# Kernel optimization log

Hardware: AMD Instinct MI355X
Metric: run time of the kernel (lower is better)

The kernel has to match this reference:

```python
import jax, jax.numpy as jnp
import numpy as np

D_MODEL = 1024
NUM_HEADS = 16
HEAD_DIM = D_MODEL // NUM_HEADS


def setup_inputs() -> dict:
    key = jax.random.key(0)
    ks = jax.random.split(key, 11)
    B, S = 2, 2048
    s = 1.0 / np.sqrt(D_MODEL)
    inp = {
        "query": jax.random.normal(ks[0], (B, S, D_MODEL), jnp.float32),
        "key": jax.random.normal(ks[1], (B, S, D_MODEL), jnp.float32),
        "value": jax.random.normal(ks[2], (B, S, D_MODEL), jnp.float32),
        "Wq": jax.random.normal(ks[3], (D_MODEL, D_MODEL), jnp.float32) * s,
        "bq": jnp.zeros((D_MODEL,), jnp.float32),
        "Wk": jax.random.normal(ks[4], (D_MODEL, D_MODEL), jnp.float32) * s,
        "bk": jnp.zeros((D_MODEL,), jnp.float32),
        "Wv": jax.random.normal(ks[5], (D_MODEL, D_MODEL), jnp.float32) * s,
        "bv": jnp.zeros((D_MODEL,), jnp.float32),
        "Wo": jax.random.normal(ks[6], (D_MODEL, D_MODEL), jnp.float32) * s,
        "bo": jnp.zeros((D_MODEL,), jnp.float32),
    }
    return inp


def _split_heads(x):
    B, S, _ = x.shape
    return x.reshape(B, S, NUM_HEADS, HEAD_DIM).transpose(0, 2, 1, 3)  # [B,H,S,d]


def reference(query, key, value, Wq, bq, Wk, bk, Wv, bv, Wo, bo):
    Q = _split_heads(query @ Wq.T + bq)
    K = _split_heads(key @ Wk.T + bk)
    V = _split_heads(value @ Wv.T + bv)
    scale = 1.0 / jnp.sqrt(jnp.asarray(HEAD_DIM, jnp.float32))
    scores = jnp.einsum("bhqd,bhkd->bhqk", Q, K) * scale  # [B,H,S,S]
    weights = jax.nn.softmax(scores, axis=-1)
    attn = jnp.einsum("bhqk,bhkd->bhqd", weights, V)
    B, H, S, d = attn.shape
    attn = attn.transpose(0, 2, 1, 3).reshape(B, S, H * d)
    return attn @ Wo.T + bo
```

## Files before the change

kernel.cpp:

```cpp
#include <hip/hip_runtime.h>
#include <hip/hip_bf16.h>


typedef unsigned short u16;
typedef __attribute__((ext_vector_type(8))) short short8;
typedef __attribute__((ext_vector_type(4))) float floatx4;

__device__ __forceinline__ float bf2f(u16 x) {
  return __uint_as_float(((unsigned)x) << 16);
}
__device__ __forceinline__ u16 f2bf(float f) {
  unsigned x = __float_as_uint(f);
  return (u16)((x + 0x7fffu + ((x >> 16) & 1u)) >> 16);
}
__device__ __forceinline__ ushort2 pk_bf16(float a, float b) {
  __hip_bfloat162 h2 = __float22bfloat162_rn(make_float2(a, b));
  ushort2 u;
  __builtin_memcpy(&u, &h2, 4);
  return u;
}
#if __has_builtin(__builtin_amdgcn_exp2f)
#define EXP2(x) __builtin_amdgcn_exp2f(x)
#else
#define EXP2(x) exp2f(x)
#endif
__device__ __forceinline__ void gll16(const u16* g, u16* lds) {
  __builtin_amdgcn_global_load_lds((const __attribute__((address_space(1))) void*)g,
                                   (__attribute__((address_space(3))) void*)lds,
                                   16, 0, 0);
}

__global__ __launch_bounds__(256) void cvt_kernel(
    const float* __restrict__ q, const float* __restrict__ k, const float* __restrict__ v,
    const float* __restrict__ wq, const float* __restrict__ wk,
    const float* __restrict__ wv, const float* __restrict__ wo,
    const float* __restrict__ bq, const float* __restrict__ bk,
    const float* __restrict__ bv, const float* __restrict__ bo,
    u16* __restrict__ ws) {
  const int i4 = (blockIdx.x * 256 + threadIdx.x) * 4;
  const float* src;
  u16* dst;
  int local;
  if (i4 < 4194304)        { src = q;  dst = ws;            local = i4; }
  else if (i4 < 8388608)   { src = k;  dst = ws + 4194304;  local = i4 - 4194304; }
  else if (i4 < 12582912)  { src = v;  dst = ws + 8388608;  local = i4 - 8388608; }
  else if (i4 < 13631488)  { src = wq; dst = ws + 12582912; local = i4 - 12582912; }
  else if (i4 < 14680064)  { src = wk; dst = ws + 13631488; local = i4 - 13631488; }
  else if (i4 < 15728640)  { src = wv; dst = ws + 14680064; local = i4 - 14680064; }
  else if (i4 < 16777216)  { src = wo; dst = ws + 15728640; local = i4 - 15728640; }
  else if (i4 < 16778240)  { src = bq; dst = ws + 16777216; local = i4 - 16777216; }
  else if (i4 < 16779264)  { src = bk; dst = ws + 16779264; local = i4 - 16778240; }
  else if (i4 < 16780288)  { src = bv; dst = ws + 16781312; local = i4 - 16779264; }
  else                     { src = bo; dst = ws + 16783360; local = i4 - 16780288; }
  const float4 f = *(const float4*)(src + local);
  ushort4 o;
  o.x = f2bf(f.x); o.y = f2bf(f.y); o.z = f2bf(f.z); o.w = f2bf(f.w);
  *(ushort4*)(dst + local) = o;
}

template <int MTILE>
__device__ __forceinline__ void gemm_tile(
    const u16* __restrict__ X, const u16* __restrict__ W,
    const u16* __restrict__ bias, u16* __restrict__ out16, float* __restrict__ out32,
    int row0, int col0, int mode, float oscale, u16* As, u16* Bs) {
  constexpr int NI = MTILE / 32;
  constexpr int ABUF = MTILE * 32;
  const int tid = threadIdx.x;
  const int w = tid >> 6, l = tid & 63;
  const int lan = l & 15, quad = l >> 4;
  const int wm = w & 1, wn = w >> 1;

  floatx4 acc[NI][4];
#pragma unroll
  for (int i = 0; i < NI; ++i)
#pragma unroll
    for (int j = 0; j < 4; ++j) acc[i][j] = (floatx4)0.0f;

  const int r0 = tid >> 2, kq0 = tid & 3;
  const int r1 = (tid + 256) >> 2;
  const int woff = w * 512;
  const u16* Xa0 = X + (size_t)(row0 + r0) * 1024 + kq0 * 8;
  const u16* Xa1 = X + (size_t)(row0 + (MTILE == 128 ? r1 : r0)) * 1024 + kq0 * 8;
  const u16* Wb0 = W + (size_t)(col0 + r0) * 1024 + kq0 * 8;
  const u16* Wb1 = W + (size_t)(col0 + r1) * 1024 + kq0 * 8;

#define STAGE(buf, kt)                                           \
  do {                                                           \
    gll16(Xa0 + (kt) * 32, As + (buf) * ABUF + woff);            \
    if (MTILE == 128)                                            \
      gll16(Xa1 + (kt) * 32, As + (buf) * ABUF + 2048 + woff);   \
    gll16(Wb0 + (kt) * 32, Bs + (buf) * 4096 + woff);            \
    gll16(Wb1 + (kt) * 32, Bs + (buf) * 4096 + 2048 + woff);     \
  } while (0)

  STAGE(0, 0);
  int cur = 0;
  for (int kt = 0; kt < 32; ++kt) {
    if (kt < 31) {
      const int nb = cur == 2 ? 0 : cur + 1;
      STAGE(nb, kt + 1);
      if (MTILE == 128)
        __asm__ volatile("s_waitcnt vmcnt(4)" ::: "memory");
      else
        __asm__ volatile("s_waitcnt vmcnt(3)" ::: "memory");
    } else {
      __asm__ volatile("s_waitcnt vmcnt(0)" ::: "memory");
    }
    __builtin_amdgcn_s_barrier();

    const u16* Ab = As + cur * ABUF;
    const u16* Bb = Bs + cur * 4096;
    short8 af[NI], bfr[4];
#pragma unroll
    for (int i = 0; i < NI; ++i)
      af[i] = *(const short8*)(Ab + (wm * (MTILE / 2) + i * 16 + lan) * 32 + quad * 8);
#pragma unroll
    for (int j = 0; j < 4; ++j)
      bfr[j] = *(const short8*)(Bb + (wn * 64 + j * 16 + lan) * 32 + quad * 8);
#pragma unroll
    for (int i = 0; i < NI; ++i)
#pragma unroll
      for (int j = 0; j < 4; ++j)
        acc[i][j] = __builtin_amdgcn_mfma_f32_16x16x32_bf16(af[i], bfr[j], acc[i][j], 0, 0, 0);
    cur = cur == 2 ? 0 : cur + 1;
  }
#undef STAGE

#pragma unroll
  for (int i = 0; i < NI; ++i) {
    const int mb = row0 + wm * (MTILE / 2) + i * 16 + quad * 4;
#pragma unroll
    for (int j = 0; j < 4; ++j) {
      const int n = col0 + wn * 64 + j * 16 + lan;
      const float bv = bf2f(bias[n]);
      if (mode == 0) {
#pragma unroll
        for (int r = 0; r < 4; ++r)
          out16[(size_t)(mb + r) * 1024 + n] = f2bf((acc[i][j][r] + bv) * oscale);
      } else if (mode == 1) {
        const int b = mb >> 11;
        const int h = n >> 6, dd = n & 63;
        u16* base = out16 + (size_t)((b * 16 + h) * 64 + dd) * 2048;
        const int s0 = mb & 2047;
        const int k0 = s0 & 63;
        const int sp0 = (s0 & ~63) | (((k0 >> 4) & 1) << 5) | (((k0 >> 2) & 3) << 3) |
                        (((k0 >> 5) & 1) << 2);
        ushort4 ov;
        ov.x = f2bf(acc[i][j][0] + bv);
        ov.y = f2bf(acc[i][j][1] + bv);
        ov.z = f2bf(acc[i][j][2] + bv);
        ov.w = f2bf(acc[i][j][3] + bv);
        *(ushort4*)(base + sp0) = ov;
      } else {
#pragma unroll
        for (int r = 0; r < 4; ++r)
          out32[(size_t)(mb + r) * 1024 + n] = acc[i][j][r] + bv;
      }
    }
  }
}

__global__ __launch_bounds__(256) void qkv_kernel(
    const u16* __restrict__ xq, const u16* __restrict__ xk, const u16* __restrict__ xv,
    const u16* __restrict__ Wq, const u16* __restrict__ Wk, const u16* __restrict__ Wv,
    const u16* __restrict__ bq, const u16* __restrict__ bk, const u16* __restrict__ bv,
    u16* __restrict__ Qo, u16* __restrict__ Ko, u16* __restrict__ Vto) {
  __shared__ __align__(16) u16 As[3 * 4096];
  __shared__ __align__(16) u16 Bs[3 * 4096];
  const int bx = blockIdx.x;
  const int xcd = bx & 7;
  const int j = bx >> 3;
  const int c = j & 7;
  const int gidx = j >> 3;
  const int g = gidx * 8 + xcd;
  const int which = g >> 5;
  const int tile_m = g & 31;
  const int col0 = c * 128;
  const u16* X = which == 0 ? xq : (which == 1 ? xk : xv);
  const u16* W = which == 0 ? Wq : (which == 1 ? Wk : Wv);
  const u16* bias = which == 0 ? bq : (which == 1 ? bk : bv);
  u16* out = which == 0 ? Qo : (which == 1 ? Ko : Vto);
  const float C = 0.125f * 1.4426950408889634f;
  gemm_tile<128>(X, W, bias, out, nullptr, tile_m * 128, col0, which == 2 ? 1 : 0,
                 which == 0 ? C : 1.0f, As, Bs);
}

__global__ __launch_bounds__(256) void proj_kernel(
    const u16* __restrict__ X, const u16* __restrict__ W,
    const u16* __restrict__ bias, float* __restrict__ out) {
  __shared__ __align__(16) u16 As[3 * 2048];
  __shared__ __align__(16) u16 Bs[3 * 4096];
  const int bx = blockIdx.x;
  const int xcd = bx & 7;
  const int j = bx >> 3;
  const int c = j & 7;
  const int gidx = j >> 3;
  const int tm = xcd * 8 + gidx;
  gemm_tile<64>(X, W, bias, nullptr, out, tm * 64, c * 128, 2, 1.0f, As, Bs);
}

#define FIXMAX 16.0f
#define KPAD 72
__global__ __launch_bounds__(256, 2) void attn_kernel(
    const u16* __restrict__ Q, const u16* __restrict__ K,
    const u16* __restrict__ Vt, u16* __restrict__ O) {
  __shared__ __align__(16) u16 KV[4][64 * KPAD];
  const int tid = threadIdx.x;
  const int w = tid >> 6, l = tid & 63;
  const int lan = l & 15, quad = l >> 4;
  const int g = w >> 1;
  const int par = w & 1;
  const int id = blockIdx.x + (blockIdx.y << 4);
  const int xcd = id & 7;
  const int jj = id >> 3;
  const int bh = xcd * 4 + (jj >> 4);
  const int q0 = (jj & 15) * 128;
  const int b = bh >> 4, h = bh & 15;
  const u16* Qg = Q + (size_t)(b * 2048 + q0) * 1024 + h * 64;
  const u16* Kg = K + (size_t)(b * 2048) * 1024 + h * 64;
  const u16* Vg = Vt + (size_t)((b * 16 + h) * 64) * 2048;

  short8 qf[4][2];
#pragma unroll
  for (int mi = 0; mi < 4; ++mi)
#pragma unroll
    for (int kk = 0; kk < 2; ++kk)
      qf[mi][kk] = *(const short8*)(Qg + (size_t)(g * 64 + mi * 16 + lan) * 1024 +
                                    kk * 32 + quad * 8);

  float lrun[4] = {0.f, 0.f, 0.f, 0.f};
  floatx4 oacc[4][4];
#pragma unroll
  for (int mi = 0; mi < 4; ++mi)
#pragma unroll
    for (int nd = 0; nd < 4; ++nd) oacc[mi][nd] = (floatx4)0.0f;

  const int rowA = tid >> 3, colq = (tid & 7) * 8;
  const int rowB = rowA + 32;

  short8 k0 = *(const short8*)(Kg + (size_t)rowA * 1024 + colq);
  short8 k1 = *(const short8*)(Kg + (size_t)rowB * 1024 + colq);
  short8 v0 = *(const short8*)(Vg + (size_t)rowA * 2048 + colq);
  short8 v1 = *(const short8*)(Vg + (size_t)rowB * 2048 + colq);
  *(short8*)(KV[0] + rowA * KPAD + colq) = k0;
  *(short8*)(KV[0] + rowB * KPAD + colq) = k1;
  *(short8*)(KV[2] + rowA * KPAD + colq) = v0;
  *(short8*)(KV[2] + rowB * KPAD + colq) = v1;
  __syncthreads();

  for (int kt = 0; kt < 32; ++kt) {
    const int cur = kt & 1;
    if (kt < 31) {
      const int kn = kt + 1;
      k0 = *(const short8*)(Kg + (size_t)(kn * 64 + rowA) * 1024 + colq);
      k1 = *(const short8*)(Kg + (size_t)(kn * 64 + rowB) * 1024 + colq);
      v0 = *(const short8*)(Vg + (size_t)rowA * 2048 + kn * 64 + colq);
      v1 = *(const short8*)(Vg + (size_t)rowB * 2048 + kn * 64 + colq);
    }

    if ((kt & 1) == par) {
      const u16* Kc = KV[cur];
      const u16* Vc = KV[2 + cur];

      floatx4 sacc[4][4];
#pragma unroll
      for (int mi = 0; mi < 4; ++mi)
#pragma unroll
        for (int nj = 0; nj < 4; ++nj) sacc[mi][nj] = (floatx4)(-FIXMAX);
#pragma unroll
      for (int kk = 0; kk < 2; ++kk) {
        short8 kf[4];
#pragma unroll
        for (int nj = 0; nj < 4; ++nj)
          kf[nj] = *(const short8*)(Kc + (nj * 16 + lan) * KPAD + kk * 32 + quad * 8);
        __builtin_amdgcn_s_setprio(1);
#pragma unroll
        for (int mi = 0; mi < 4; ++mi)
#pragma unroll
          for (int nj = 0; nj < 4; ++nj)
            sacc[mi][nj] = __builtin_amdgcn_mfma_f32_16x16x32_bf16(
                kf[nj], qf[mi][kk], sacc[mi][nj], 0, 0, 0);
        __builtin_amdgcn_s_setprio(0);
      }

      short8 pb[4][2];
#pragma unroll
      for (int mi = 0; mi < 4; ++mi) {
        float p[4][4];
#pragma unroll
        for (int nj = 0; nj < 4; ++nj)
#pragma unroll
          for (int r = 0; r < 4; ++r) p[nj][r] = EXP2(sacc[mi][nj][r]);
        float s01 = 0.f, s23 = 0.f;
#pragma unroll
        for (int r = 0; r < 4; ++r) {
          s01 += p[0][r] + p[1][r];
          s23 += p[2][r] + p[3][r];
        }
        lrun[mi] += s01 + s23;
#pragma unroll
        for (int kk = 0; kk < 2; ++kk) {
          const ushort2 w0 = pk_bf16(p[kk][0], p[kk][1]);
          const ushort2 w1 = pk_bf16(p[kk][2], p[kk][3]);
          const ushort2 w2 = pk_bf16(p[kk + 2][0], p[kk + 2][1]);
          const ushort2 w3 = pk_bf16(p[kk + 2][2], p[kk + 2][3]);
          union { short8 s8; ushort us[8]; } u;
          u.us[0] = w0.x; u.us[1] = w0.y; u.us[2] = w1.x; u.us[3] = w1.y;
          u.us[4] = w2.x; u.us[5] = w2.y; u.us[6] = w3.x; u.us[7] = w3.y;
          pb[mi][kk] = u.s8;
        }
      }

#pragma unroll
      for (int kk = 0; kk < 2; ++kk) {
        short8 vf[4];
#pragma unroll
        for (int nd = 0; nd < 4; ++nd)
          vf[nd] = *(const short8*)(Vc + (nd * 16 + lan) * KPAD + kk * 32 + quad * 8);
        __builtin_amdgcn_s_setprio(1);
#pragma unroll
        for (int mi = 0; mi < 4; ++mi)
#pragma unroll
          for (int nd = 0; nd < 4; ++nd)
            oacc[mi][nd] = __builtin_amdgcn_mfma_f32_16x16x32_bf16(
                vf[nd], pb[mi][kk], oacc[mi][nd], 0, 0, 0);
        __builtin_amdgcn_s_setprio(0);
      }
    }

    if (kt < 31) {
      const int nxt = cur ^ 1;
      *(short8*)(KV[nxt] + rowA * KPAD + colq) = k0;
      *(short8*)(KV[nxt] + rowB * KPAD + colq) = k1;
      *(short8*)(KV[2 + nxt] + rowA * KPAD + colq) = v0;
      *(short8*)(KV[2 + nxt] + rowB * KPAD + colq) = v1;
      __syncthreads();
    }
  }

#pragma unroll
  for (int mi = 0; mi < 4; ++mi) {
    lrun[mi] += __shfl_xor(lrun[mi], 16);
    lrun[mi] += __shfl_xor(lrun[mi], 32);
  }
  __syncthreads();
  float4* obuf = (float4*)&KV[0][0];
  float* lbuf = (float*)&KV[0][0] + 8192;
  if (par == 1) {
#pragma unroll
    for (int mi = 0; mi < 4; ++mi) {
#pragma unroll
      for (int nd = 0; nd < 4; ++nd) {
        const int fi = mi * 4 + nd;
        float4 t;
        t.x = oacc[mi][nd][0]; t.y = oacc[mi][nd][1];
        t.z = oacc[mi][nd][2]; t.w = oacc[mi][nd][3];
        obuf[(g * 64 + l) * 16 + ((fi + l) & 15)] = t;
      }
      lbuf[(g * 64 + l) * 4 + mi] = lrun[mi];
    }
  }
  __syncthreads();
  if (par == 0) {
#pragma unroll
    for (int mi = 0; mi < 4; ++mi) {
      const float lt = lrun[mi] + lbuf[(g * 64 + l) * 4 + mi];
      const float inv = 1.0f / lt;
      const int qg = b * 2048 + q0 + g * 64 + mi * 16 + lan;
#pragma unroll
      for (int nd = 0; nd < 4; ++nd) {
        const int fi = mi * 4 + nd;
        const float4 t = obuf[(g * 64 + l) * 16 + ((fi + l) & 15)];
        ushort4 ov;
        ov.x = f2bf((oacc[mi][nd][0] + t.x) * inv);
        ov.y = f2bf((oacc[mi][nd][1] + t.y) * inv);
        ov.z = f2bf((oacc[mi][nd][2] + t.z) * inv);
        ov.w = f2bf((oacc[mi][nd][3] + t.w) * inv);
        *(ushort4*)(O + (size_t)qg * 1024 + h * 64 + nd * 16 + quad * 4) = ov;
      }
    }
  }
}

extern "C" void kernel_launch(void* const* d_in, const int* in_sizes, int n_in,
                              void* d_out, int out_size, void* d_ws, size_t ws_size,
                              hipStream_t stream) {
  const float* query = (const float*)d_in[0];
  const float* key_ = (const float*)d_in[1];
  const float* value = (const float*)d_in[2];
  const float* Wq = (const float*)d_in[3];
  const float* bq = (const float*)d_in[4];
  const float* Wk = (const float*)d_in[5];
  const float* bk = (const float*)d_in[6];
  const float* Wv = (const float*)d_in[7];
  const float* bv = (const float*)d_in[8];
  const float* Wo = (const float*)d_in[9];
  const float* bo = (const float*)d_in[10];
  float* out = (float*)d_out;

  u16* ws = (u16*)d_ws;
  u16* Xq = ws;
  u16* Xk = ws + 4194304;
  u16* Xv = ws + 8388608;
  u16* cWq = ws + 12582912;
  u16* cWk = ws + 13631488;
  u16* cWv = ws + 14680064;
  u16* cWo = ws + 15728640;
  u16* cbq = ws + 16777216;
  u16* cbk = ws + 16779264;
  u16* cbv = ws + 16781312;
  u16* cbo = ws + 16783360;
  u16* Qw = ws + 17301504;
  u16* Kw = ws + 21495808;
  u16* Vtw = ws + 25690112;
  u16* Ow = ws + 29884416;

  cvt_kernel<<<16388, 256, 0, stream>>>(query, key_, value, Wq, Wk, Wv, Wo,
                                        bq, bk, bv, bo, ws);
  qkv_kernel<<<768, 256, 0, stream>>>(Xq, Xk, Xv, cWq, cWk, cWv, cbq, cbk, cbv,
                                      Qw, Kw, Vtw);
  attn_kernel<<<dim3(16, 32), 256, 0, stream>>>(Qw, Kw, Vtw, Ow);
  proj_kernel<<<512, 256, 0, stream>>>(Ow, cWo, cbo, out);
}
```

Baseline: 222.1 us.

## Split each KV tile across wave pair by key halves instead of alternating tiles

Before, the two waves in a pair took alternate KV tiles, so each wave sat idle on every other iteration. Now both waves work on every tile, and each handles half of the 64 keys: 32 keys for QK^T and the matching 32-key slice of V for PV. The V layout permutation in the QKV projection's output is changed so that one 32-element slice of V matches the packed P fragment. Total MFMA work per wave stays the same, but it is spread evenly across iterations, which should overlap better with the loads. The price is a full QK/exp/PV pass per iteration with smaller MFMA batches for each wave.

```diff
diff --git a/kernel.cpp b/kernel.cpp
--- a/kernel.cpp
+++ b/kernel.cpp
@@ -143,8 +143,8 @@
         u16* base = out16 + (size_t)((b * 16 + h) * 64 + dd) * 2048;
         const int s0 = mb & 2047;
         const int k0 = s0 & 63;
-        const int sp0 = (s0 & ~63) | (((k0 >> 4) & 1) << 5) | (((k0 >> 2) & 3) << 3) |
-                        (((k0 >> 5) & 1) << 2);
+        const int sp0 = (s0 & ~63) | (((k0 >> 5) & 1) << 5) | (((k0 >> 2) & 3) << 3) |
+                        (((k0 >> 4) & 1) << 2);
         ushort4 ov;
         ov.x = f2bf(acc[i][j][0] + bv);
         ov.y = f2bf(acc[i][j][1] + bv);
@@ -209,7 +209,7 @@
   const int w = tid >> 6, l = tid & 63;
   const int lan = l & 15, quad = l >> 4;
   const int g = w >> 1;
-  const int par = w & 1;
+  const int h2 = w & 1;
   const int id = blockIdx.x + (blockIdx.y << 4);
   const int xcd = id & 7;
   const int jj = id >> 3;
@@ -257,76 +257,69 @@
       v0 = *(const short8*)(Vg + (size_t)rowA * 2048 + kn * 64 + colq);
       v1 = *(const short8*)(Vg + (size_t)rowB * 2048 + kn * 64 + colq);
     }
-
-    if ((kt & 1) == par) {
-      const u16* Kc = KV[cur];
-      const u16* Vc = KV[2 + cur];
-
-      floatx4 sacc[4][4];
+    const u16* Kc = KV[cur];
+    const u16* Vc = KV[2 + cur];
+
+    floatx4 sacc[4][2];
+#pragma unroll
+    for (int mi = 0; mi < 4; ++mi)
+#pragma unroll
+      for (int nj2 = 0; nj2 < 2; ++nj2) sacc[mi][nj2] = (floatx4)(-FIXMAX);
+#pragma unroll
+    for (int kk = 0; kk < 2; ++kk) {
+      short8 kf[2];
+#pragma unroll
+      for (int nj2 = 0; nj2 < 2; ++nj2)
+        kf[nj2] = *(const short8*)(Kc + ((2 * h2 + nj2) * 16 + lan) * KPAD +
+                                   kk * 32 + quad * 8);
+      __builtin_amdgcn_s_setprio(1);
 #pragma unroll
       for (int mi = 0; mi < 4; ++mi)
 #pragma unroll
-        for (int nj = 0; nj < 4; ++nj) sacc[mi][nj] = (floatx4)(-FIXMAX);
-#pragma unroll
-      for (int kk = 0; kk < 2; ++kk) {
-        short8 kf[4];
-#pragma unroll
-        for (int nj = 0; nj < 4; ++nj)
-          kf[nj] = *(const short8*)(Kc + (nj * 16 + lan) * KPAD + kk * 32 + quad * 8);
-        __builtin_amdgcn_s_setprio(1);
-#pragma unroll
-        for (int mi = 0; mi < 4; ++mi)
-#pragma unroll
-          for (int nj = 0; nj < 4; ++nj)
-            sacc[mi][nj] = __builtin_amdgcn_mfma_f32_16x16x32_bf16(
-                kf[nj], qf[mi][kk], sacc[mi][nj], 0, 0, 0);
-        __builtin_amdgcn_s_setprio(0);
+        for (int nj2 = 0; nj2 < 2; ++nj2)
+          sacc[mi][nj2] = __builtin_amdgcn_mfma_f32_16x16x32_bf16(
+              kf[nj2], qf[mi][kk], sacc[mi][nj2], 0, 0, 0);
+      __builtin_amdgcn_s_setprio(0);
+    }
+
+    short8 vf[4];
+#pragma unroll
+    for (int nd = 0; nd < 4; ++nd)
+      vf[nd] = *(const short8*)(Vc + (nd * 16 + lan) * KPAD + h2 * 32 + quad * 8);
+
+    short8 pb[4];
+#pragma unroll
+    for (int mi = 0; mi < 4; ++mi) {
+      float p[2][4];
+#pragma unroll
+      for (int nj2 = 0; nj2 < 2; ++nj2)
+#pragma unroll
+        for (int r = 0; r < 4; ++r) p[nj2][r] = EXP2(sacc[mi][nj2][r]);
+      float s0 = 0.f, s1 = 0.f;
+#pragma unroll
+      for (int r = 0; r < 4; ++r) {
+        s0 += p[0][r];
+        s1 += p[1][r];
       }
-
-      short8 pb[4][2];
-#pragma unroll
-      for (int mi = 0; mi < 4; ++mi) {
-        float p[4][4];
-#pragma unroll
-        for (int nj = 0; nj < 4; ++nj)
-#pragma unroll
-          for (int r = 0; r < 4; ++r) p[nj][r] = EXP2(sacc[mi][nj][r]);
-        float s01 = 0.f, s23 = 0.f;
-#pragma unroll
-        for (int r = 0; r < 4; ++r) {
-          s01 += p[0][r] + p[1][r];
-          s23 += p[2][r] + p[3][r];
-        }
-        lrun[mi] += s01 + s23;
-#pragma unroll
-        for (int kk = 0; kk < 2; ++kk) {
-          const ushort2 w0 = pk_bf16(p[kk][0], p[kk][1]);
-          const ushort2 w1 = pk_bf16(p[kk][2], p[kk][3]);
-          const ushort2 w2 = pk_bf16(p[kk + 2][0], p[kk + 2][1]);
-          const ushort2 w3 = pk_bf16(p[kk + 2][2], p[kk + 2][3]);
-          union { short8 s8; ushort us[8]; } u;
-          u.us[0] = w0.x; u.us[1] = w0.y; u.us[2] = w1.x; u.us[3] = w1.y;
-          u.us[4] = w2.x; u.us[5] = w2.y; u.us[6] = w3.x; u.us[7] = w3.y;
-          pb[mi][kk] = u.s8;
-        }
-      }
-
-#pragma unroll
-      for (int kk = 0; kk < 2; ++kk) {
-        short8 vf[4];
-#pragma unroll
-        for (int nd = 0; nd < 4; ++nd)
-          vf[nd] = *(const short8*)(Vc + (nd * 16 + lan) * KPAD + kk * 32 + quad * 8);
-        __builtin_amdgcn_s_setprio(1);
-#pragma unroll
-        for (int mi = 0; mi < 4; ++mi)
-#pragma unroll
-          for (int nd = 0; nd < 4; ++nd)
-            oacc[mi][nd] = __builtin_amdgcn_mfma_f32_16x16x32_bf16(
-                vf[nd], pb[mi][kk], oacc[mi][nd], 0, 0, 0);
-        __builtin_amdgcn_s_setprio(0);
-      }
-    }
+      lrun[mi] += s0 + s1;
+      const ushort2 w0 = pk_bf16(p[0][0], p[0][1]);
+      const ushort2 w1 = pk_bf16(p[0][2], p[0][3]);
+      const ushort2 w2 = pk_bf16(p[1][0], p[1][1]);
+      const ushort2 w3 = pk_bf16(p[1][2], p[1][3]);
+      union { short8 s8; ushort us[8]; } u;
+      u.us[0] = w0.x; u.us[1] = w0.y; u.us[2] = w1.x; u.us[3] = w1.y;
+      u.us[4] = w2.x; u.us[5] = w2.y; u.us[6] = w3.x; u.us[7] = w3.y;
+      pb[mi] = u.s8;
+    }
+
+    __builtin_amdgcn_s_setprio(1);
+#pragma unroll
+    for (int mi = 0; mi < 4; ++mi)
+#pragma unroll
+      for (int nd = 0; nd < 4; ++nd)
+        oacc[mi][nd] = __builtin_amdgcn_mfma_f32_16x16x32_bf16(
+            vf[nd], pb[mi], oacc[mi][nd], 0, 0, 0);
+    __builtin_amdgcn_s_setprio(0);
 
     if (kt < 31) {
       const int nxt = cur ^ 1;
@@ -346,7 +339,7 @@
   __syncthreads();
   float4* obuf = (float4*)&KV[0][0];
   float* lbuf = (float*)&KV[0][0] + 8192;
-  if (par == 1) {
+  if (h2 == 1) {
 #pragma unroll
     for (int mi = 0; mi < 4; ++mi) {
 #pragma unroll
@@ -361,7 +354,7 @@
     }
   }
   __syncthreads();
-  if (par == 0) {
+  if (h2 == 0) {
 #pragma unroll
     for (int mi = 0; mi < 4; ++mi) {
       const float lt = lrun[mi] + lbuf[(g * 64 + l) * 4 + mi];
```

Result: faster. 217.7 us (median of 2 runs) (-2.0%).
